# Optimization experiments

Hardware: AMD Instinct MI355X
Metric: run time of the kernel (lower is better)

## Reference

```python
import jax, jax.numpy as jnp
import numpy as np

OUT_DIM = 64
NUM_HEADS = 8
HID = NUM_HEADS * OUT_DIM  # 512
ALPHA = 0.01  # leaky relu slope
N_NODES = 20000
N_EDGES = 100000
MP_LEN = 3


def setup_inputs() -> dict:
    key = jax.random.key(0)
    ks = jax.random.split(key, 8)
    s = 1.0 / np.sqrt(HID)
    return {
        "features": jax.random.normal(ks[0], (N_NODES, OUT_DIM), jnp.float32),
        "W_ih": jax.random.normal(ks[1], (3 * HID, OUT_DIM), jnp.float32) * s,
        "W_hh": jax.random.normal(ks[2], (3 * HID, HID), jnp.float32) * s,
        "b_ih": jax.random.normal(ks[3], (3 * HID,), jnp.float32) * s,
        "b_hh": jax.random.normal(ks[4], (3 * HID,), jnp.float32) * s,
        "attn": jax.random.normal(ks[5], (NUM_HEADS, OUT_DIM), jnp.float32) * 0.1,
        "edge_metapath_indices": jax.random.randint(ks[6], (N_EDGES, MP_LEN), 0, N_NODES),
        "edge_dst": jax.random.randint(ks[7], (N_EDGES,), 0, N_NODES),
    }


def _gru_last_hidden(x_seq, W_ih, W_hh, b_ih, b_hh):
    """x_seq: [L, E, D] -> final hidden [E, HID] (torch nn.GRU math, h0=0)."""
    E = x_seq.shape[1]
    h0 = jnp.zeros((E, HID), x_seq.dtype)

    def step(h, x):
        gi = x @ W_ih.T + b_ih  # [E, 3*HID]
        gh = h @ W_hh.T + b_hh  # [E, 3*HID]
        i_r, i_z, i_n = jnp.split(gi, 3, axis=-1)
        h_r, h_z, h_n = jnp.split(gh, 3, axis=-1)
        r = jax.nn.sigmoid(i_r + h_r)
        z = jax.nn.sigmoid(i_z + h_z)
        n = jnp.tanh(i_n + r * h_n)
        h_new = (1.0 - z) * n + z * h
        return h_new, None

    h_last, _ = jax.lax.scan(step, h0, x_seq)
    return h_last


def reference(features, W_ih, W_hh, b_ih, b_hh, attn,
              edge_metapath_indices, edge_dst):
    N = features.shape[0]
    # gather metapath node features: [E, L, D] -> GRU over L
    edata = features[edge_metapath_indices]
    h = _gru_last_hidden(jnp.transpose(edata, (1, 0, 2)), W_ih, W_hh, b_ih, b_hh)
    eft = h.reshape(-1, NUM_HEADS, OUT_DIM)  # [E, H, D]
    # attention logits per edge/head + leaky relu
    a = jnp.sum(eft * attn[None], axis=-1)  # [E, H]
    a = jnp.where(a >= 0, a, ALPHA * a)
    # edge softmax grouped by destination node
    amax = jax.ops.segment_max(a, edge_dst, num_segments=N)  # [N, H]
    ea = jnp.exp(a - amax[edge_dst])
    denom = jax.ops.segment_sum(ea, edge_dst, num_segments=N)  # [N, H]
    alpha = ea / denom[edge_dst]  # [E, H]
    # weighted message aggregation (sum) to destination nodes
    msg = eft * alpha[:, :, None]  # [E, H, D]
    ret = jax.ops.segment_sum(msg, edge_dst, num_segments=N)  # [N, H, D]
    return ret
```

## Files before the change

### kernel.cpp

```cpp
#include <hip/hip_runtime.h>
#include <hip/hip_bf16.h>

#define N_NODES 20000
#define N_EDGES 100000
#define HID 512
#define G3 1536
#define NH 8
#define OD 64

typedef __hip_bfloat16 bf16;
typedef __attribute__((ext_vector_type(8))) short bf16x8;
typedef __attribute__((ext_vector_type(4))) float f32x4;

__device__ __forceinline__ float frcp(float x) { return __builtin_amdgcn_rcpf(x); }
__device__ __forceinline__ float fsig(float x) { return frcp(1.0f + __expf(-x)); }
__device__ __forceinline__ float ftanh(float x) { return 1.0f - 2.0f * frcp(__expf(2.0f * x) + 1.0f); }
__device__ __forceinline__ float b2f(bf16 b) { return __bfloat162float(b); }
__device__ __forceinline__ bf16 f2b(float f) { return __float2bfloat16(f); }
__device__ __forceinline__ float bs2f(short s) {
    return __uint_as_float(((unsigned)(unsigned short)s) << 16);
}
__device__ __forceinline__ float us2f(unsigned short s) {
    return __uint_as_float(((unsigned)s) << 16);
}
__device__ __forceinline__ short f2bs(float f) {
    bf16 b = __float2bfloat16(f);
    return *reinterpret_cast<short*>(&b);
}
__device__ __forceinline__ unsigned ford(float f) {
    unsigned u = __float_as_uint(f);
    return (u & 0x80000000u) ? ~u : (u | 0x80000000u);
}
__device__ __forceinline__ float iford(unsigned u) {
    return __uint_as_float((u & 0x80000000u) ? (u & 0x7fffffffu) : ~u);
}

__device__ __forceinline__ void g2l16(const void* g, void* l) {
#if __has_builtin(__builtin_amdgcn_global_load_lds)
    __builtin_amdgcn_global_load_lds((const __attribute__((address_space(1))) char*)g,
                                     (__attribute__((address_space(3))) char*)l, 16, 0, 0);
#else
    *(bf16x8*)l = *(const bf16x8*)g;
#endif
}


__global__ __launch_bounds__(256) void k_prep(const float* __restrict__ Whh,
                                              const float* __restrict__ Wih,
                                              bf16* __restrict__ WTs,
                                              float* __restrict__ WIT) {
    int t = blockIdx.x * 256 + threadIdx.x;
    if (t < 98304) {
        int T = t >> 10, c = (t >> 6) & 15, l = t & 63;
        int n = T * 16 + (l & 15);
        int k = c * 32 + ((l >> 4) << 3);
        const float* src = Whh + (size_t)n * 512 + k;
        bf16x8 v;
#pragma unroll
        for (int j = 0; j < 8; ++j) v[j] = f2bs(src[j]);
        *(bf16x8*)(WTs + (size_t)t * 8) = v;
    } else {
        int u = t - 98304;
        int d = u / 1536, j = u % 1536;
        WIT[u] = Wih[(size_t)j * 64 + d];
    }
}

__global__ __launch_bounds__(256) void k_count(const int* __restrict__ dst,
                                               unsigned* __restrict__ cnt) {
    int e = blockIdx.x * 256 + threadIdx.x;
    if (e < N_EDGES) atomicAdd(&cnt[dst[e]], 1u);
}

#define SCAN_CH 79
__global__ __launch_bounds__(256) void k_scan(const unsigned* __restrict__ cnt,
                                              unsigned* __restrict__ base,
                                              unsigned* __restrict__ cursor) {
    __shared__ unsigned ls[256];
    int t = threadIdx.x;
    int s0 = t * SCAN_CH;
    int s1 = s0 + SCAN_CH < N_NODES ? s0 + SCAN_CH : N_NODES;
    unsigned s = 0;
    for (int i = s0; i < s1; ++i) s += cnt[i];
    ls[t] = s;
    __syncthreads();
    for (int d = 1; d < 256; d <<= 1) {
        unsigned v = (t >= d) ? ls[t - d] : 0u;
        __syncthreads();
        ls[t] += v;
        __syncthreads();
    }
    unsigned run = ls[t] - s;
    for (int i = s0; i < s1; ++i) {
        base[i] = run; cursor[i] = run; run += cnt[i];
    }
    if (t == 255) base[N_NODES] = ls[255];
}

__global__ __launch_bounds__(256) void k_fill(const int* __restrict__ dst,
                                              unsigned* __restrict__ cursor,
                                              unsigned* __restrict__ csr) {
    int e = blockIdx.x * 256 + threadIdx.x;
    if (e < N_EDGES) {
        unsigned p = atomicAdd(&cursor[dst[e]], 1u);
        csr[p] = (unsigned)e;
    }
}

__global__ __launch_bounds__(256) void k_gi(const float* __restrict__ feat,
                                            const float* __restrict__ WIT,
                                            const float* __restrict__ b_ih,
                                            const float* __restrict__ b_hh,
                                            bf16* __restrict__ G,
                                            bf16* __restrict__ H1) {
    __shared__ float fs[16][64];
    const int n0 = blockIdx.x * 16;
    const int k = blockIdx.y * 256 + threadIdx.x;
    for (int i = threadIdx.x; i < 16 * 64; i += 256)
        fs[0][i] = feat[(size_t)n0 * 64 + i];
    __syncthreads();
    float acc[3][16];
#pragma unroll
    for (int g = 0; g < 3; ++g) {
        float b = b_ih[g * 512 + k];
#pragma unroll
        for (int e = 0; e < 16; ++e) acc[g][e] = b;
    }
    for (int d = 0; d < 64; d += 4) {
        float w[3][4];
#pragma unroll
        for (int u = 0; u < 4; ++u)
#pragma unroll
            for (int g = 0; g < 3; ++g)
                w[g][u] = WIT[(size_t)(d + u) * G3 + g * 512 + k];
#pragma unroll
        for (int e = 0; e < 16; ++e) {
            float4 f = *(const float4*)&fs[e][d];
#pragma unroll
            for (int g = 0; g < 3; ++g)
                acc[g][e] += w[g][0] * f.x + w[g][1] * f.y + w[g][2] * f.z + w[g][3] * f.w;
        }
    }
    const float br = b_hh[k], bz = b_hh[512 + k], bn = b_hh[1024 + k];
#pragma unroll
    for (int e = 0; e < 16; ++e) {
        bf16* dst = G + (size_t)(n0 + e) * G3 + k * 3;
        dst[0] = f2b(acc[0][e]);
        dst[1] = f2b(acc[1][e]);
        dst[2] = f2b(acc[2][e]);
        float r1 = fsig(acc[0][e] + br);
        float z1 = fsig(acc[1][e] + bz);
        float n1 = ftanh(acc[2][e] + r1 * bn);
        H1[(size_t)(n0 + e) * HID + k] = f2b((1.0f - z1) * n1);
    }
}

__global__ __launch_bounds__(256, 2) void k_gh2(const bf16* __restrict__ H1,
                                                const bf16* __restrict__ WTs,
                                                const float* __restrict__ b_hh,
                                                bf16* __restrict__ GH2) {
    __shared__ short Bs[2][8192];
    const int tid = threadIdx.x;
    const int wave = tid >> 6, lane = tid & 63;
    const int m0 = blockIdx.x * 128;
    const int k0 = (lane >> 4) << 3;

    bf16x8 afrag[2][16];
#pragma unroll
    for (int t = 0; t < 2; ++t) {
        int row = m0 + wave * 32 + t * 16 + (lane & 15);
        int ar = row < N_NODES ? row : N_NODES - 1;
#pragma unroll
        for (int c = 0; c < 16; ++c)
            afrag[t][c] = *(const bf16x8*)(H1 + (size_t)ar * HID + c * 32 + k0);
    }

    const int col = lane & 15;
    const int qb = (lane >> 4) << 2;
    const int boff = lane * 8;

#pragma unroll
    for (int i = 0; i < 4; ++i) {
        int q = tid + i * 256;
        g2l16(WTs + (size_t)q * 8, &Bs[0][q * 8]);
    }
    __syncthreads();

    int cur = 0;
    for (int jt = 0; jt < 32; ++jt) {
        const int cj = jt * 16 + col;
        f32x4 acc[2][3];
#pragma unroll
        for (int t = 0; t < 2; ++t)
#pragma unroll
            for (int g = 0; g < 3; ++g) acc[t][g] = (f32x4){0, 0, 0, 0};
        const float br = b_hh[cj], bz = b_hh[512 + cj], bn = b_hh[1024 + cj];
        {
#pragma unroll
            for (int i = 0; i < 4; ++i) {
                int q = tid + i * 256;
                g2l16(WTs + 262144 + (size_t)jt * 8192 + q * 8, &Bs[cur ^ 1][q * 8]);
            }
            const short* cb = &Bs[cur][0];
#pragma unroll
            for (int c = 0; c < 16; ++c) {
                bf16x8 b = *(const bf16x8*)&cb[c * 512 + boff];
                acc[0][0] = __builtin_amdgcn_mfma_f32_16x16x32_bf16(afrag[0][c], b, acc[0][0], 0, 0, 0);
                acc[1][0] = __builtin_amdgcn_mfma_f32_16x16x32_bf16(afrag[1][c], b, acc[1][0], 0, 0, 0);
            }
            __syncthreads();
            cur ^= 1;
        }
        {
#pragma unroll
            for (int i = 0; i < 4; ++i) {
                int q = tid + i * 256;
                g2l16(WTs + 524288 + (size_t)jt * 8192 + q * 8, &Bs[cur ^ 1][q * 8]);
            }
            const short* cb = &Bs[cur][0];
#pragma unroll
            for (int c = 0; c < 16; ++c) {
                bf16x8 b = *(const bf16x8*)&cb[c * 512 + boff];
                acc[0][1] = __builtin_amdgcn_mfma_f32_16x16x32_bf16(afrag[0][c], b, acc[0][1], 0, 0, 0);
                acc[1][1] = __builtin_amdgcn_mfma_f32_16x16x32_bf16(afrag[1][c], b, acc[1][1], 0, 0, 0);
            }
            __syncthreads();
            cur ^= 1;
        }
        {
            if (jt < 31) {
#pragma unroll
                for (int i = 0; i < 4; ++i) {
                    int q = tid + i * 256;
                    g2l16(WTs + (size_t)(jt + 1) * 8192 + q * 8, &Bs[cur ^ 1][q * 8]);
                }
            }
            const short* cb = &Bs[cur][0];
#pragma unroll
            for (int c = 0; c < 16; ++c) {
                bf16x8 b = *(const bf16x8*)&cb[c * 512 + boff];
                acc[0][2] = __builtin_amdgcn_mfma_f32_16x16x32_bf16(afrag[0][c], b, acc[0][2], 0, 0, 0);
                acc[1][2] = __builtin_amdgcn_mfma_f32_16x16x32_bf16(afrag[1][c], b, acc[1][2], 0, 0, 0);
            }
#pragma unroll
            for (int t = 0; t < 2; ++t)
#pragma unroll
                for (int q = 0; q < 4; ++q) {
                    int e = m0 + wave * 32 + t * 16 + qb + q;
                    if (e < N_NODES) {
                        bf16* dst = GH2 + (size_t)e * G3 + cj * 3;
                        dst[0] = f2b(acc[t][0][q] + br);
                        dst[1] = f2b(acc[t][1][q] + bz);
                        dst[2] = f2b(acc[t][2][q] + bn);
                    }
                }
            __syncthreads();
            cur ^= 1;
        }
    }
}

__global__ __launch_bounds__(256) void k_h2(const bf16* __restrict__ G,
                                            const bf16* __restrict__ GH2,
                                            const bf16* __restrict__ H1,
                                            const int* __restrict__ emi,
                                            bf16* __restrict__ h2) {
    size_t i = (size_t)blockIdx.x * 256 + threadIdx.x;
    int e = (int)(i >> 6);
    int kc = (int)(i & 63) * 8;
    int i0 = emi[(size_t)e * 3 + 0];
    int i1 = emi[(size_t)e * 3 + 1];
    const bf16* g1p = G + (size_t)i1 * G3 + kc * 3;
    const bf16* ghp = GH2 + (size_t)i0 * G3 + kc * 3;
    bf16x8 h1v = *(const bf16x8*)(H1 + (size_t)i0 * HID + kc);
    short s1[24], sh[24];
    {
        bf16x8 a0 = *(const bf16x8*)g1p, a1 = *(const bf16x8*)(g1p + 8), a2 = *(const bf16x8*)(g1p + 16);
        bf16x8 c0 = *(const bf16x8*)ghp, c1 = *(const bf16x8*)(ghp + 8), c2 = *(const bf16x8*)(ghp + 16);
#pragma unroll
        for (int j = 0; j < 8; ++j) {
            s1[j] = a0[j]; s1[8 + j] = a1[j]; s1[16 + j] = a2[j];
            sh[j] = c0[j]; sh[8 + j] = c1[j]; sh[16 + j] = c2[j];
        }
    }
    bf16x8 out;
#pragma unroll
    for (int j = 0; j < 8; ++j) {
        float r = fsig(bs2f(s1[j * 3 + 0]) + bs2f(sh[j * 3 + 0]));
        float z = fsig(bs2f(s1[j * 3 + 1]) + bs2f(sh[j * 3 + 1]));
        float n = ftanh(bs2f(s1[j * 3 + 2]) + r * bs2f(sh[j * 3 + 2]));
        out[j] = f2bs((1.0f - z) * n + z * bs2f(h1v[j]));
    }
    *(bf16x8*)(h2 + (size_t)e * HID + kc) = out;
}

__global__ __launch_bounds__(256, 2) void k_gemm3(const bf16* __restrict__ G,
                                                  const bf16* __restrict__ WTs,
                                                  const float* __restrict__ b_hh,
                                                  const int* __restrict__ emi,
                                                  bf16* __restrict__ h2) {
    __shared__ short Bs[2][8192];
    __shared__ int si2[128];
    const int tid = threadIdx.x;
    const int wave = tid >> 6, lane = tid & 63;
    const int m0 = blockIdx.x * 128;
    if (tid < 128) {
        int e = m0 + tid;
        si2[tid] = emi[(size_t)(e < N_EDGES ? e : N_EDGES - 1) * 3 + 2];
    }
    const int k0 = (lane >> 4) << 3;

    bf16x8 afrag[2][16];
#pragma unroll
    for (int t = 0; t < 2; ++t) {
        int row = m0 + wave * 32 + t * 16 + (lane & 15);
        int ar = row < N_EDGES ? row : N_EDGES - 1;
#pragma unroll
        for (int c = 0; c < 16; ++c)
            afrag[t][c] = *(const bf16x8*)(h2 + (size_t)ar * HID + c * 32 + k0);
    }

    const int col = lane & 15;
    const int qb = (lane >> 4) << 2;
    const int boff = lane * 8;

#pragma unroll
    for (int i = 0; i < 4; ++i) {
        int q = tid + i * 256;
        g2l16(WTs + (size_t)q * 8, &Bs[0][q * 8]);
    }
    __syncthreads();

    int cur = 0;
    for (int jt = 0; jt < 32; ++jt) {
        const int cj = jt * 16 + col;
        f32x4 acc[2][3];
#pragma unroll
        for (int t = 0; t < 2; ++t)
#pragma unroll
            for (int g = 0; g < 3; ++g) acc[t][g] = (f32x4){0, 0, 0, 0};
        float br, bz, bn;
        unsigned short pg[2][4][3], ph[2][4];
        {
            br = b_hh[cj]; bz = b_hh[512 + cj]; bn = b_hh[1024 + cj];
#pragma unroll
            for (int t = 0; t < 2; ++t)
#pragma unroll
                for (int q = 0; q < 4; ++q) {
                    int li = wave * 32 + t * 16 + qb + q;
                    int e = m0 + li;
                    int ec = e < N_EDGES ? e : N_EDGES - 1;
                    const unsigned short* g2p =
                        (const unsigned short*)(G + (size_t)si2[li] * G3 + cj * 3);
                    pg[t][q][0] = g2p[0]; pg[t][q][1] = g2p[1]; pg[t][q][2] = g2p[2];
                    ph[t][q] = ((const unsigned short*)h2)[(size_t)ec * HID + cj];
                }
#pragma unroll
            for (int i = 0; i < 4; ++i) {
                int q = tid + i * 256;
                g2l16(WTs + 262144 + (size_t)jt * 8192 + q * 8, &Bs[cur ^ 1][q * 8]);
            }
            const short* cb = &Bs[cur][0];
#pragma unroll
            for (int c = 0; c < 16; ++c) {
                bf16x8 b = *(const bf16x8*)&cb[c * 512 + boff];
                acc[0][0] = __builtin_amdgcn_mfma_f32_16x16x32_bf16(afrag[0][c], b, acc[0][0], 0, 0, 0);
                acc[1][0] = __builtin_amdgcn_mfma_f32_16x16x32_bf16(afrag[1][c], b, acc[1][0], 0, 0, 0);
            }
            __syncthreads();
            cur ^= 1;
        }
        {
#pragma unroll
            for (int i = 0; i < 4; ++i) {
                int q = tid + i * 256;
                g2l16(WTs + 524288 + (size_t)jt * 8192 + q * 8, &Bs[cur ^ 1][q * 8]);
            }
            const short* cb = &Bs[cur][0];
#pragma unroll
            for (int c = 0; c < 16; ++c) {
                bf16x8 b = *(const bf16x8*)&cb[c * 512 + boff];
                acc[0][1] = __builtin_amdgcn_mfma_f32_16x16x32_bf16(afrag[0][c], b, acc[0][1], 0, 0, 0);
                acc[1][1] = __builtin_amdgcn_mfma_f32_16x16x32_bf16(afrag[1][c], b, acc[1][1], 0, 0, 0);
            }
            __syncthreads();
            cur ^= 1;
        }
        {
            if (jt < 31) {
#pragma unroll
                for (int i = 0; i < 4; ++i) {
                    int q = tid + i * 256;
                    g2l16(WTs + (size_t)(jt + 1) * 8192 + q * 8, &Bs[cur ^ 1][q * 8]);
                }
            }
            const short* cb = &Bs[cur][0];
#pragma unroll
            for (int c = 0; c < 16; ++c) {
                bf16x8 b = *(const bf16x8*)&cb[c * 512 + boff];
                acc[0][2] = __builtin_amdgcn_mfma_f32_16x16x32_bf16(afrag[0][c], b, acc[0][2], 0, 0, 0);
                acc[1][2] = __builtin_amdgcn_mfma_f32_16x16x32_bf16(afrag[1][c], b, acc[1][2], 0, 0, 0);
            }
#pragma unroll
            for (int t = 0; t < 2; ++t)
#pragma unroll
                for (int q = 0; q < 4; ++q) {
                    int e = m0 + wave * 32 + t * 16 + qb + q;
                    if (e < N_EDGES) {
                        float r = fsig(us2f(pg[t][q][0]) + acc[t][0][q] + br);
                        float z = fsig(us2f(pg[t][q][1]) + acc[t][1][q] + bz);
                        float ng = ftanh(us2f(pg[t][q][2]) + r * (acc[t][2][q] + bn));
                        h2[(size_t)e * HID + cj] = f2b((1.0f - z) * ng + z * us2f(ph[t][q]));
                    }
                }
            __syncthreads();
            cur ^= 1;
        }
    }
}

__global__ __launch_bounds__(256) void k_logits(const bf16* __restrict__ eft,
                                                const float* __restrict__ attn,
                                                const int* __restrict__ dst,
                                                float* __restrict__ a,
                                                unsigned* __restrict__ amax) {
    int i = blockIdx.x * 256 + threadIdx.x;
    int e = i >> 3, h = i & 7;
    const __hip_bfloat162* f2 = (const __hip_bfloat162*)(eft + (size_t)e * HID + h * OD);
    const float* at = attn + h * OD;
    float s = 0.f;
#pragma unroll
    for (int d = 0; d < OD / 2; ++d) {
        float2 fv = __bfloat1622float2(f2[d]);
        s += fv.x * at[2 * d] + fv.y * at[2 * d + 1];
    }
    s = (s >= 0.f) ? s : 0.01f * s;
    a[i] = s;
    atomicMax(&amax[(size_t)dst[e] * NH + h], ford(s));
}

__global__ __launch_bounds__(256) void k_ea(const int* __restrict__ dst,
                                            const unsigned* __restrict__ amax,
                                            float* __restrict__ a,
                                            float* __restrict__ denom) {
    int i = blockIdx.x * 256 + threadIdx.x;
    int e = i >> 3, h = i & 7;
    float m = iford(amax[(size_t)dst[e] * NH + h]);
    float v = __expf(a[i] - m);
    a[i] = v;
    atomicAdd(&denom[(size_t)dst[e] * NH + h], v);
}

__global__ __launch_bounds__(256) void k_out(const bf16* __restrict__ eft,
                                             const float* __restrict__ a,
                                             const float* __restrict__ denom,
                                             const unsigned* __restrict__ base,
                                             const unsigned* __restrict__ csr,
                                             float* __restrict__ out) {
    int n = blockIdx.x;
    int k = blockIdx.y * 256 + threadIdx.x;
    int h = k >> 6;
    unsigned b0 = base[n], b1 = base[n + 1];
    float rden = (b1 > b0) ? frcp(denom[(size_t)n * NH + h]) : 0.0f;
    float acc = 0.f;
    for (unsigned i = b0; i < b1; ++i) {
        unsigned e = csr[i];
        float al = a[(size_t)e * NH + h];
        acc += b2f(eft[(size_t)e * HID + k]) * al;
    }
    out[(size_t)n * HID + k] = acc * rden;
}

extern "C" void kernel_launch(void* const* d_in, const int* in_sizes, int n_in,
                              void* d_out, int out_size, void* d_ws, size_t ws_size,
                              hipStream_t stream) {
    (void)in_sizes; (void)n_in; (void)ws_size; (void)out_size;
    const float* feat = (const float*)d_in[0];
    const float* W_ih = (const float*)d_in[1];
    const float* W_hh = (const float*)d_in[2];
    const float* b_ih = (const float*)d_in[3];
    const float* b_hh = (const float*)d_in[4];
    const float* attn = (const float*)d_in[5];
    const int* emi = (const int*)d_in[6];
    const int* dst = (const int*)d_in[7];
    float* out = (float*)d_out;

    char* ws = (char*)d_ws;
    bf16* G = (bf16*)ws;
    bf16* GH2 = (bf16*)(ws + 61440000);
    bf16* h2 = (bf16*)(ws + 122880000);
    bf16* WTs = (bf16*)(ws + 225280000);
    float* WIT = (float*)(ws + 226852864);
    float* a = (float*)(ws + 227246080);
    unsigned* amax = (unsigned*)(ws + 230446080);
    float* denom = (float*)(ws + 231086080);
    unsigned* cnt = (unsigned*)(ws + 231726080);
    unsigned* base = (unsigned*)(ws + 231806080);
    unsigned* cursor = (unsigned*)(ws + 231886088);
    unsigned* csr = (unsigned*)(ws + 231966088);
    bf16* H1 = (bf16*)(ws + 232366088);

    (void)hipMemsetAsync(amax, 0, 1360000, stream);

    k_prep<<<768, 256, 0, stream>>>(W_hh, W_ih, WTs, WIT);
    k_count<<<391, 256, 0, stream>>>(dst, cnt);
    k_scan<<<1, 256, 0, stream>>>(cnt, base, cursor);
    k_fill<<<391, 256, 0, stream>>>(dst, cursor, csr);
    k_gi<<<dim3(1250, 2), 256, 0, stream>>>(feat, WIT, b_ih, b_hh, G, H1);
    k_gh2<<<157, 256, 0, stream>>>(H1, WTs, b_hh, GH2);
    k_h2<<<25000, 256, 0, stream>>>(G, GH2, H1, emi, h2);
    k_gemm3<<<782, 256, 0, stream>>>(G, WTs, b_hh, emi, h2);
    k_logits<<<3125, 256, 0, stream>>>(h2, attn, dst, a, amax);
    k_ea<<<3125, 256, 0, stream>>>(dst, amax, a, denom);
    k_out<<<dim3(N_NODES, 2), 256, 0, stream>>>(h2, a, denom, base, csr, out);
}
```

Before: 801.4 us.

## Fuse input-gate GEMM into final GRU step and shrink tile to 64 rows

The third GRU step no longer gathers its precomputed input-gate values from the G table. It now computes x@W_ih on the fly with two extra MFMAs per gate, using bf16 copies of the features and of a swizzled W_ih prepared in k_prep. The per-block edge tile drops from 128 to 64 rows and the occupancy hint rises from 2 to 3 blocks, which reduces register pressure from the A fragments. In exchange there is extra MFMA work and B-tile reloads are amortised over fewer rows, while the scattered 2-byte gathers from the large G table go away.

```diff
diff --git a/kernel.cpp b/kernel.cpp
--- a/kernel.cpp
+++ b/kernel.cpp
@@ -47,7 +47,10 @@
 
 __global__ __launch_bounds__(256) void k_prep(const float* __restrict__ Whh,
                                               const float* __restrict__ Wih,
+                                              const float* __restrict__ feat,
                                               bf16* __restrict__ WTs,
+                                              bf16* __restrict__ WIE,
+                                              bf16* __restrict__ featB,
                                               float* __restrict__ WIT) {
     int t = blockIdx.x * 256 + threadIdx.x;
     if (t < 98304) {
@@ -59,10 +62,27 @@
 #pragma unroll
         for (int j = 0; j < 8; ++j) v[j] = f2bs(src[j]);
         *(bf16x8*)(WTs + (size_t)t * 8) = v;
-    } else {
+    } else if (t < 196608) {
         int u = t - 98304;
         int d = u / 1536, j = u % 1536;
         WIT[u] = Wih[(size_t)j * 64 + d];
+    } else if (t < 208896) {
+        int u = t - 196608;
+        int l = u & 63, cc = (u >> 6) & 1, jt = (u >> 7) & 31, g = u >> 12;
+        int row = g * 512 + jt * 16 + (l & 15);
+        int d0 = cc * 32 + ((l >> 4) << 3);
+        const float* src = Wih + (size_t)row * 64 + d0;
+        bf16x8 v;
+#pragma unroll
+        for (int j = 0; j < 8; ++j) v[j] = f2bs(src[j]);
+        *(bf16x8*)(WIE + (size_t)u * 8) = v;
+    } else {
+        int u = t - 208896;
+        const float* src = feat + (size_t)u * 8;
+        bf16x8 v;
+#pragma unroll
+        for (int j = 0; j < 8; ++j) v[j] = f2bs(src[j]);
+        *(bf16x8*)(featB + (size_t)u * 8) = v;
     }
 }
 
@@ -294,32 +314,23 @@
     *(bf16x8*)(h2 + (size_t)e * HID + kc) = out;
 }
 
-__global__ __launch_bounds__(256, 2) void k_gemm3(const bf16* __restrict__ G,
+__global__ __launch_bounds__(256, 3) void k_gemm3(const bf16* __restrict__ featB,
                                                   const bf16* __restrict__ WTs,
+                                                  const bf16* __restrict__ WIE,
+                                                  const float* __restrict__ b_ih,
                                                   const float* __restrict__ b_hh,
                                                   const int* __restrict__ emi,
                                                   bf16* __restrict__ h2) {
-    __shared__ short Bs[2][8192];
-    __shared__ int si2[128];
+    __shared__ short Bs[2][9216];
+    __shared__ int si2[64];
     const int tid = threadIdx.x;
     const int wave = tid >> 6, lane = tid & 63;
-    const int m0 = blockIdx.x * 128;
-    if (tid < 128) {
+    const int m0 = blockIdx.x * 64;
+    if (tid < 64) {
         int e = m0 + tid;
         si2[tid] = emi[(size_t)(e < N_EDGES ? e : N_EDGES - 1) * 3 + 2];
     }
     const int k0 = (lane >> 4) << 3;
-
-    bf16x8 afrag[2][16];
-#pragma unroll
-    for (int t = 0; t < 2; ++t) {
-        int row = m0 + wave * 32 + t * 16 + (lane & 15);
-        int ar = row < N_EDGES ? row : N_EDGES - 1;
-#pragma unroll
-        for (int c = 0; c < 16; ++c)
-            afrag[t][c] = *(const bf16x8*)(h2 + (size_t)ar * HID + c * 32 + k0);
-    }
-
     const int col = lane & 15;
     const int qb = (lane >> 4) << 2;
     const int boff = lane * 8;
@@ -329,43 +340,55 @@
         int q = tid + i * 256;
         g2l16(WTs + (size_t)q * 8, &Bs[0][q * 8]);
     }
+    if (tid < 128) g2l16(WIE + (size_t)tid * 8, &Bs[0][8192 + tid * 8]);
     __syncthreads();
+
+    bf16x8 afrag[18];
+    {
+        int row = m0 + wave * 16 + (lane & 15);
+        int ar = row < N_EDGES ? row : N_EDGES - 1;
+#pragma unroll
+        for (int c = 0; c < 16; ++c)
+            afrag[c] = *(const bf16x8*)(h2 + (size_t)ar * HID + c * 32 + k0);
+        int i2r = si2[wave * 16 + (lane & 15)];
+        afrag[16] = *(const bf16x8*)(featB + (size_t)i2r * 64 + k0);
+        afrag[17] = *(const bf16x8*)(featB + (size_t)i2r * 64 + 32 + k0);
+    }
 
     int cur = 0;
     for (int jt = 0; jt < 32; ++jt) {
         const int cj = jt * 16 + col;
-        f32x4 acc[2][3];
-#pragma unroll
-        for (int t = 0; t < 2; ++t)
-#pragma unroll
-            for (int g = 0; g < 3; ++g) acc[t][g] = (f32x4){0, 0, 0, 0};
-        float br, bz, bn;
-        unsigned short pg[2][4][3], ph[2][4];
+        f32x4 ar_ = {0, 0, 0, 0}, az_ = {0, 0, 0, 0};
+        f32x4 ahn = {0, 0, 0, 0}, ain = {0, 0, 0, 0};
+        float bihr, bihz, bihn, bhhr, bhhz, bhhn;
+        unsigned short ph[4];
         {
-            br = b_hh[cj]; bz = b_hh[512 + cj]; bn = b_hh[1024 + cj];
-#pragma unroll
-            for (int t = 0; t < 2; ++t)
-#pragma unroll
-                for (int q = 0; q < 4; ++q) {
-                    int li = wave * 32 + t * 16 + qb + q;
-                    int e = m0 + li;
-                    int ec = e < N_EDGES ? e : N_EDGES - 1;
-                    const unsigned short* g2p =
-                        (const unsigned short*)(G + (size_t)si2[li] * G3 + cj * 3);
-                    pg[t][q][0] = g2p[0]; pg[t][q][1] = g2p[1]; pg[t][q][2] = g2p[2];
-                    ph[t][q] = ((const unsigned short*)h2)[(size_t)ec * HID + cj];
-                }
+            bihr = b_ih[cj]; bihz = b_ih[512 + cj]; bihn = b_ih[1024 + cj];
+            bhhr = b_hh[cj]; bhhz = b_hh[512 + cj]; bhhn = b_hh[1024 + cj];
+#pragma unroll
+            for (int q = 0; q < 4; ++q) {
+                int e = m0 + wave * 16 + qb + q;
+                int ec = e < N_EDGES ? e : N_EDGES - 1;
+                ph[q] = ((const unsigned short*)h2)[(size_t)ec * HID + cj];
+            }
 #pragma unroll
             for (int i = 0; i < 4; ++i) {
                 int q = tid + i * 256;
                 g2l16(WTs + 262144 + (size_t)jt * 8192 + q * 8, &Bs[cur ^ 1][q * 8]);
             }
+            if (tid < 128)
+                g2l16(WIE + 32768 + (size_t)jt * 1024 + tid * 8, &Bs[cur ^ 1][8192 + tid * 8]);
             const short* cb = &Bs[cur][0];
 #pragma unroll
             for (int c = 0; c < 16; ++c) {
                 bf16x8 b = *(const bf16x8*)&cb[c * 512 + boff];
-                acc[0][0] = __builtin_amdgcn_mfma_f32_16x16x32_bf16(afrag[0][c], b, acc[0][0], 0, 0, 0);
-                acc[1][0] = __builtin_amdgcn_mfma_f32_16x16x32_bf16(afrag[1][c], b, acc[1][0], 0, 0, 0);
+                ar_ = __builtin_amdgcn_mfma_f32_16x16x32_bf16(afrag[c], b, ar_, 0, 0, 0);
+            }
+            {
+                bf16x8 b16 = *(const bf16x8*)&cb[8192 + boff];
+                bf16x8 b17 = *(const bf16x8*)&cb[8192 + 512 + boff];
+                ar_ = __builtin_amdgcn_mfma_f32_16x16x32_bf16(afrag[16], b16, ar_, 0, 0, 0);
+                ar_ = __builtin_amdgcn_mfma_f32_16x16x32_bf16(afrag[17], b17, ar_, 0, 0, 0);
             }
             __syncthreads();
             cur ^= 1;
@@ -376,12 +399,19 @@
                 int q = tid + i * 256;
                 g2l16(WTs + 524288 + (size_t)jt * 8192 + q * 8, &Bs[cur ^ 1][q * 8]);
             }
+            if (tid < 128)
+                g2l16(WIE + 65536 + (size_t)jt * 1024 + tid * 8, &Bs[cur ^ 1][8192 + tid * 8]);
             const short* cb = &Bs[cur][0];
 #pragma unroll
             for (int c = 0; c < 16; ++c) {
                 bf16x8 b = *(const bf16x8*)&cb[c * 512 + boff];
-                acc[0][1] = __builtin_amdgcn_mfma_f32_16x16x32_bf16(afrag[0][c], b, acc[0][1], 0, 0, 0);
-                acc[1][1] = __builtin_amdgcn_mfma_f32_16x16x32_bf16(afrag[1][c], b, acc[1][1], 0, 0, 0);
+                az_ = __builtin_amdgcn_mfma_f32_16x16x32_bf16(afrag[c], b, az_, 0, 0, 0);
+            }
+            {
+                bf16x8 b16 = *(const bf16x8*)&cb[8192 + boff];
+                bf16x8 b17 = *(const bf16x8*)&cb[8192 + 512 + boff];
+                az_ = __builtin_amdgcn_mfma_f32_16x16x32_bf16(afrag[16], b16, az_, 0, 0, 0);
+                az_ = __builtin_amdgcn_mfma_f32_16x16x32_bf16(afrag[17], b17, az_, 0, 0, 0);
             }
             __syncthreads();
             cur ^= 1;
@@ -393,26 +423,31 @@
                     int q = tid + i * 256;
                     g2l16(WTs + (size_t)(jt + 1) * 8192 + q * 8, &Bs[cur ^ 1][q * 8]);
                 }
+                if (tid < 128)
+                    g2l16(WIE + (size_t)(jt + 1) * 1024 + tid * 8, &Bs[cur ^ 1][8192 + tid * 8]);
             }
             const short* cb = &Bs[cur][0];
 #pragma unroll
             for (int c = 0; c < 16; ++c) {
                 bf16x8 b = *(const bf16x8*)&cb[c * 512 + boff];
-                acc[0][2] = __builtin_amdgcn_mfma_f32_16x16x32_bf16(afrag[0][c], b, acc[0][2], 0, 0, 0);
-                acc[1][2] = __builtin_amdgcn_mfma_f32_16x16x32_bf16(afrag[1][c], b, acc[1][2], 0, 0, 0);
-            }
-#pragma unroll
-            for (int t = 0; t < 2; ++t)
-#pragma unroll
-                for (int q = 0; q < 4; ++q) {
-                    int e = m0 + wave * 32 + t * 16 + qb + q;
-                    if (e < N_EDGES) {
-                        float r = fsig(us2f(pg[t][q][0]) + acc[t][0][q] + br);
-                        float z = fsig(us2f(pg[t][q][1]) + acc[t][1][q] + bz);
-                        float ng = ftanh(us2f(pg[t][q][2]) + r * (acc[t][2][q] + bn));
-                        h2[(size_t)e * HID + cj] = f2b((1.0f - z) * ng + z * us2f(ph[t][q]));
-                    }
+                ahn = __builtin_amdgcn_mfma_f32_16x16x32_bf16(afrag[c], b, ahn, 0, 0, 0);
+            }
+            {
+                bf16x8 b16 = *(const bf16x8*)&cb[8192 + boff];
+                bf16x8 b17 = *(const bf16x8*)&cb[8192 + 512 + boff];
+                ain = __builtin_amdgcn_mfma_f32_16x16x32_bf16(afrag[16], b16, ain, 0, 0, 0);
+                ain = __builtin_amdgcn_mfma_f32_16x16x32_bf16(afrag[17], b17, ain, 0, 0, 0);
+            }
+#pragma unroll
+            for (int q = 0; q < 4; ++q) {
+                int e = m0 + wave * 16 + qb + q;
+                if (e < N_EDGES) {
+                    float r = fsig(ar_[q] + bihr + bhhr);
+                    float z = fsig(az_[q] + bihz + bhhz);
+                    float n = ftanh(ain[q] + bihn + r * (ahn[q] + bhhn));
+                    h2[(size_t)e * HID + cj] = f2b((1.0f - z) * n + z * us2f(ph[q]));
                 }
+            }
             __syncthreads();
             cur ^= 1;
         }
@@ -499,17 +534,19 @@
     unsigned* cursor = (unsigned*)(ws + 231886088);
     unsigned* csr = (unsigned*)(ws + 231966088);
     bf16* H1 = (bf16*)(ws + 232366088);
+    bf16* WIE = (bf16*)(ws + 227246080);
+    bf16* featB = (bf16*)(ws + 227442688);
 
     (void)hipMemsetAsync(amax, 0, 1360000, stream);
 
-    k_prep<<<768, 256, 0, stream>>>(W_hh, W_ih, WTs, WIT);
+    k_prep<<<1441, 256, 0, stream>>>(W_hh, W_ih, feat, WTs, WIE, featB, WIT);
     k_count<<<391, 256, 0, stream>>>(dst, cnt);
     k_scan<<<1, 256, 0, stream>>>(cnt, base, cursor);
     k_fill<<<391, 256, 0, stream>>>(dst, cursor, csr);
     k_gi<<<dim3(1250, 2), 256, 0, stream>>>(feat, WIT, b_ih, b_hh, G, H1);
     k_gh2<<<157, 256, 0, stream>>>(H1, WTs, b_hh, GH2);
     k_h2<<<25000, 256, 0, stream>>>(G, GH2, H1, emi, h2);
-    k_gemm3<<<782, 256, 0, stream>>>(G, WTs, b_hh, emi, h2);
+    k_gemm3<<<1563, 256, 0, stream>>>(featB, WTs, WIE, b_ih, b_hh, emi, h2);
     k_logits<<<3125, 256, 0, stream>>>(h2, attn, dst, a, amax);
     k_ea<<<3125, 256, 0, stream>>>(dst, amax, a, denom);
     k_out<<<dim3(N_NODES, 2), 256, 0, stream>>>(h2, a, denom, base, csr, out);
```

After: 788.6 us. Within noise of the previous version (-1.6%).

## Restructure final GRU GEMM to keep weights resident and fuse input projection

Applied to the files above, without the earlier changes.

The third-step GEMM now gives each block a fixed 16-column slice of all three gates, keeps those W_hh and W_ih tiles resident in LDS, and loops over 33 row tiles. The input projection is computed inline with MFMA from bf16 features instead of reading the precomputed G buffer. Output goes to a separate buffer so h2 stays unchanged, and blocks are mapped to XCDs for L2 locality. The GH2 kernel now stages outputs through LDS so it can issue coalesced 16-byte stores. The cost is more LDS per block, a larger A-fragment register set, and bf16 rounding of the input projection.

```diff
diff --git a/kernel.cpp b/kernel.cpp
--- a/kernel.cpp
+++ b/kernel.cpp
@@ -47,7 +47,10 @@
 
 __global__ __launch_bounds__(256) void k_prep(const float* __restrict__ Whh,
                                               const float* __restrict__ Wih,
+                                              const float* __restrict__ feat,
                                               bf16* __restrict__ WTs,
+                                              bf16* __restrict__ WIE,
+                                              bf16* __restrict__ featB,
                                               float* __restrict__ WIT) {
     int t = blockIdx.x * 256 + threadIdx.x;
     if (t < 98304) {
@@ -59,10 +62,28 @@
 #pragma unroll
         for (int j = 0; j < 8; ++j) v[j] = f2bs(src[j]);
         *(bf16x8*)(WTs + (size_t)t * 8) = v;
-    } else {
+    } else if (t < 196608) {
         int u = t - 98304;
         int d = u / 1536, j = u % 1536;
         WIT[u] = Wih[(size_t)j * 64 + d];
+    } else if (t < 208896) {
+        int u = t - 196608;
+        int l = u & 63, cc = (u >> 6) & 1, jg = u >> 7;
+        int jt = jg & 31, g = jg >> 5;
+        int row = g * 512 + jt * 16 + (l & 15);
+        int d0 = cc * 32 + ((l >> 4) << 3);
+        const float* src = Wih + (size_t)row * 64 + d0;
+        bf16x8 v;
+#pragma unroll
+        for (int j = 0; j < 8; ++j) v[j] = f2bs(src[j]);
+        *(bf16x8*)(WIE + (size_t)u * 8) = v;
+    } else {
+        int u = t - 208896;
+        const float* src = feat + (size_t)u * 8;
+        bf16x8 v;
+#pragma unroll
+        for (int j = 0; j < 8; ++j) v[j] = f2bs(src[j]);
+        *(bf16x8*)(featB + (size_t)u * 8) = v;
     }
 }
 
@@ -160,6 +181,7 @@
                                                 const float* __restrict__ b_hh,
                                                 bf16* __restrict__ GH2) {
     __shared__ short Bs[2][8192];
+    __shared__ short tile2[128 * 48];
     const int tid = threadIdx.x;
     const int wave = tid >> 6, lane = tid & 63;
     const int m0 = blockIdx.x * 128;
@@ -196,6 +218,17 @@
             for (int g = 0; g < 3; ++g) acc[t][g] = (f32x4){0, 0, 0, 0};
         const float br = b_hh[cj], bz = b_hh[512 + cj], bn = b_hh[1024 + cj];
         {
+            if (jt > 0) {
+                int pj = jt - 1;
+#pragma unroll
+                for (int i_ = 0; i_ < 3; ++i_) {
+                    int idx = i_ * 256 + tid;
+                    int rg = m0 + (idx / 6);
+                    if (rg < N_NODES)
+                        *(bf16x8*)(GH2 + (size_t)rg * G3 + pj * 48 + (idx % 6) * 8) =
+                            *(const bf16x8*)&tile2[idx * 8];
+                }
+            }
 #pragma unroll
             for (int i = 0; i < 4; ++i) {
                 int q = tid + i * 256;
@@ -246,17 +279,23 @@
             for (int t = 0; t < 2; ++t)
 #pragma unroll
                 for (int q = 0; q < 4; ++q) {
-                    int e = m0 + wave * 32 + t * 16 + qb + q;
-                    if (e < N_NODES) {
-                        bf16* dst = GH2 + (size_t)e * G3 + cj * 3;
-                        dst[0] = f2b(acc[t][0][q] + br);
-                        dst[1] = f2b(acc[t][1][q] + bz);
-                        dst[2] = f2b(acc[t][2][q] + bn);
-                    }
+                    int lr = wave * 32 + t * 16 + qb + q;
+                    short* s = &tile2[lr * 48 + col * 3];
+                    s[0] = f2bs(acc[t][0][q] + br);
+                    s[1] = f2bs(acc[t][1][q] + bz);
+                    s[2] = f2bs(acc[t][2][q] + bn);
                 }
             __syncthreads();
             cur ^= 1;
         }
+    }
+#pragma unroll
+    for (int i_ = 0; i_ < 3; ++i_) {
+        int idx = i_ * 256 + tid;
+        int rg = m0 + (idx / 6);
+        if (rg < N_NODES)
+            *(bf16x8*)(GH2 + (size_t)rg * G3 + 31 * 48 + (idx % 6) * 8) =
+                *(const bf16x8*)&tile2[idx * 8];
     }
 }
 
@@ -294,128 +333,111 @@
     *(bf16x8*)(h2 + (size_t)e * HID + kc) = out;
 }
 
-__global__ __launch_bounds__(256, 2) void k_gemm3(const bf16* __restrict__ G,
+__global__ __launch_bounds__(256, 2) void k_gemm3(const bf16* __restrict__ featB,
                                                   const bf16* __restrict__ WTs,
+                                                  const bf16* __restrict__ WIE,
+                                                  const float* __restrict__ b_ih,
                                                   const float* __restrict__ b_hh,
                                                   const int* __restrict__ emi,
-                                                  bf16* __restrict__ h2) {
-    __shared__ short Bs[2][8192];
-    __shared__ int si2[128];
+                                                  const bf16* __restrict__ h2,
+                                                  bf16* __restrict__ h3out) {
+    __shared__ short Ws[3][8192];
+    __shared__ short We[3][1024];
     const int tid = threadIdx.x;
     const int wave = tid >> 6, lane = tid & 63;
-    const int m0 = blockIdx.x * 128;
-    if (tid < 128) {
-        int e = m0 + tid;
-        si2[tid] = emi[(size_t)(e < N_EDGES ? e : N_EDGES - 1) * 3 + 2];
-    }
+    const int bid = blockIdx.x;
+    const int xcd = bid & 7, sl = bid >> 3;
+    const int mt = xcd * 3 + (sl >> 5);
+    const int cg = sl & 31;
+    const int mbase = mt * 4224;
+    const int col = lane & 15;
+    const int cj = cg * 16 + col;
     const int k0 = (lane >> 4) << 3;
-
-    bf16x8 afrag[2][16];
-#pragma unroll
-    for (int t = 0; t < 2; ++t) {
-        int row = m0 + wave * 32 + t * 16 + (lane & 15);
-        int ar = row < N_EDGES ? row : N_EDGES - 1;
-#pragma unroll
-        for (int c = 0; c < 16; ++c)
-            afrag[t][c] = *(const bf16x8*)(h2 + (size_t)ar * HID + c * 32 + k0);
-    }
-
-    const int col = lane & 15;
     const int qb = (lane >> 4) << 2;
     const int boff = lane * 8;
 
 #pragma unroll
-    for (int i = 0; i < 4; ++i) {
-        int q = tid + i * 256;
-        g2l16(WTs + (size_t)q * 8, &Bs[0][q * 8]);
-    }
+    for (int g = 0; g < 3; ++g) {
+#pragma unroll
+        for (int i = 0; i < 4; ++i) {
+            int q = tid + i * 256;
+            g2l16(WTs + (size_t)g * 262144 + (size_t)cg * 8192 + q * 8, &Ws[g][q * 8]);
+        }
+        if (tid < 128)
+            g2l16(WIE + (size_t)g * 32768 + (size_t)cg * 1024 + tid * 8, &We[g][tid * 8]);
+    }
+    const float rb = b_ih[cj] + b_hh[cj];
+    const float zb = b_ih[512 + cj] + b_hh[512 + cj];
+    const float nb = b_ih[1024 + cj];
+    const float hb = b_hh[1024 + cj];
     __syncthreads();
 
-    int cur = 0;
-    for (int jt = 0; jt < 32; ++jt) {
-        const int cj = jt * 16 + col;
-        f32x4 acc[2][3];
+    for (int st = 0; st < 33; ++st) {
+        const int rowb = mbase + st * 128 + wave * 32;
+        bf16x8 af[2][18];
+#pragma unroll
+        for (int t = 0; t < 2; ++t) {
+            int row = rowb + t * 16 + (lane & 15);
+            int ar = row < N_EDGES ? row : N_EDGES - 1;
+#pragma unroll
+            for (int c = 0; c < 16; ++c)
+                af[t][c] = *(const bf16x8*)(h2 + (size_t)ar * HID + c * 32 + k0);
+            int i2 = emi[(size_t)ar * 3 + 2];
+            af[t][16] = *(const bf16x8*)(featB + (size_t)i2 * 64 + k0);
+            af[t][17] = *(const bf16x8*)(featB + (size_t)i2 * 64 + 32 + k0);
+        }
+        unsigned short ph[2][4];
 #pragma unroll
         for (int t = 0; t < 2; ++t)
 #pragma unroll
-            for (int g = 0; g < 3; ++g) acc[t][g] = (f32x4){0, 0, 0, 0};
-        float br, bz, bn;
-        unsigned short pg[2][4][3], ph[2][4];
-        {
-            br = b_hh[cj]; bz = b_hh[512 + cj]; bn = b_hh[1024 + cj];
-#pragma unroll
-            for (int t = 0; t < 2; ++t)
-#pragma unroll
-                for (int q = 0; q < 4; ++q) {
-                    int li = wave * 32 + t * 16 + qb + q;
-                    int e = m0 + li;
-                    int ec = e < N_EDGES ? e : N_EDGES - 1;
-                    const unsigned short* g2p =
-                        (const unsigned short*)(G + (size_t)si2[li] * G3 + cj * 3);
-                    pg[t][q][0] = g2p[0]; pg[t][q][1] = g2p[1]; pg[t][q][2] = g2p[2];
-                    ph[t][q] = ((const unsigned short*)h2)[(size_t)ec * HID + cj];
+            for (int q = 0; q < 4; ++q) {
+                int row = rowb + t * 16 + qb + q;
+                int ec = row < N_EDGES ? row : N_EDGES - 1;
+                ph[t][q] = ((const unsigned short*)h2)[(size_t)ec * HID + cj];
+            }
+        f32x4 ar_[2], az_[2], ahn[2], ain[2];
+#pragma unroll
+        for (int t = 0; t < 2; ++t) {
+            ar_[t] = (f32x4){0, 0, 0, 0}; az_[t] = (f32x4){0, 0, 0, 0};
+            ahn[t] = (f32x4){0, 0, 0, 0}; ain[t] = (f32x4){0, 0, 0, 0};
+        }
+#pragma unroll
+        for (int c = 0; c < 16; ++c) {
+            bf16x8 br = *(const bf16x8*)&Ws[0][c * 512 + boff];
+            bf16x8 bz = *(const bf16x8*)&Ws[1][c * 512 + boff];
+            bf16x8 bn = *(const bf16x8*)&Ws[2][c * 512 + boff];
+#pragma unroll
+            for (int t = 0; t < 2; ++t) {
+                ar_[t] = __builtin_amdgcn_mfma_f32_16x16x32_bf16(af[t][c], br, ar_[t], 0, 0, 0);
+                az_[t] = __builtin_amdgcn_mfma_f32_16x16x32_bf16(af[t][c], bz, az_[t], 0, 0, 0);
+                ahn[t] = __builtin_amdgcn_mfma_f32_16x16x32_bf16(af[t][c], bn, ahn[t], 0, 0, 0);
+            }
+        }
+#pragma unroll
+        for (int cc = 0; cc < 2; ++cc) {
+            bf16x8 br = *(const bf16x8*)&We[0][cc * 512 + boff];
+            bf16x8 bz = *(const bf16x8*)&We[1][cc * 512 + boff];
+            bf16x8 bn = *(const bf16x8*)&We[2][cc * 512 + boff];
+#pragma unroll
+            for (int t = 0; t < 2; ++t) {
+                ar_[t] = __builtin_amdgcn_mfma_f32_16x16x32_bf16(af[t][16 + cc], br, ar_[t], 0, 0, 0);
+                az_[t] = __builtin_amdgcn_mfma_f32_16x16x32_bf16(af[t][16 + cc], bz, az_[t], 0, 0, 0);
+                ain[t] = __builtin_amdgcn_mfma_f32_16x16x32_bf16(af[t][16 + cc], bn, ain[t], 0, 0, 0);
+            }
+        }
+#pragma unroll
+        for (int t = 0; t < 2; ++t)
+#pragma unroll
+            for (int q = 0; q < 4; ++q) {
+                int row = rowb + t * 16 + qb + q;
+                if (row < N_EDGES) {
+                    float r = fsig(ar_[t][q] + rb);
+                    float z = fsig(az_[t][q] + zb);
+                    float n = ftanh(ain[t][q] + nb + r * (ahn[t][q] + hb));
+                    h3out[(size_t)row * HID + cj] =
+                        f2b((1.0f - z) * n + z * us2f(ph[t][q]));
                 }
-#pragma unroll
-            for (int i = 0; i < 4; ++i) {
-                int q = tid + i * 256;
-                g2l16(WTs + 262144 + (size_t)jt * 8192 + q * 8, &Bs[cur ^ 1][q * 8]);
-            }
-            const short* cb = &Bs[cur][0];
-#pragma unroll
-            for (int c = 0; c < 16; ++c) {
-                bf16x8 b = *(const bf16x8*)&cb[c * 512 + boff];
-                acc[0][0] = __builtin_amdgcn_mfma_f32_16x16x32_bf16(afrag[0][c], b, acc[0][0], 0, 0, 0);
-                acc[1][0] = __builtin_amdgcn_mfma_f32_16x16x32_bf16(afrag[1][c], b, acc[1][0], 0, 0, 0);
-            }
-            __syncthreads();
-            cur ^= 1;
-        }
-        {
-#pragma unroll
-            for (int i = 0; i < 4; ++i) {
-                int q = tid + i * 256;
-                g2l16(WTs + 524288 + (size_t)jt * 8192 + q * 8, &Bs[cur ^ 1][q * 8]);
-            }
-            const short* cb = &Bs[cur][0];
-#pragma unroll
-            for (int c = 0; c < 16; ++c) {
-                bf16x8 b = *(const bf16x8*)&cb[c * 512 + boff];
-                acc[0][1] = __builtin_amdgcn_mfma_f32_16x16x32_bf16(afrag[0][c], b, acc[0][1], 0, 0, 0);
-                acc[1][1] = __builtin_amdgcn_mfma_f32_16x16x32_bf16(afrag[1][c], b, acc[1][1], 0, 0, 0);
-            }
-            __syncthreads();
-            cur ^= 1;
-        }
-        {
-            if (jt < 31) {
-#pragma unroll
-                for (int i = 0; i < 4; ++i) {
-                    int q = tid + i * 256;
-                    g2l16(WTs + (size_t)(jt + 1) * 8192 + q * 8, &Bs[cur ^ 1][q * 8]);
-                }
-            }
-            const short* cb = &Bs[cur][0];
-#pragma unroll
-            for (int c = 0; c < 16; ++c) {
-                bf16x8 b = *(const bf16x8*)&cb[c * 512 + boff];
-                acc[0][2] = __builtin_amdgcn_mfma_f32_16x16x32_bf16(afrag[0][c], b, acc[0][2], 0, 0, 0);
-                acc[1][2] = __builtin_amdgcn_mfma_f32_16x16x32_bf16(afrag[1][c], b, acc[1][2], 0, 0, 0);
-            }
-#pragma unroll
-            for (int t = 0; t < 2; ++t)
-#pragma unroll
-                for (int q = 0; q < 4; ++q) {
-                    int e = m0 + wave * 32 + t * 16 + qb + q;
-                    if (e < N_EDGES) {
-                        float r = fsig(us2f(pg[t][q][0]) + acc[t][0][q] + br);
-                        float z = fsig(us2f(pg[t][q][1]) + acc[t][1][q] + bz);
-                        float ng = ftanh(us2f(pg[t][q][2]) + r * (acc[t][2][q] + bn));
-                        h2[(size_t)e * HID + cj] = f2b((1.0f - z) * ng + z * us2f(ph[t][q]));
-                    }
-                }
-            __syncthreads();
-            cur ^= 1;
-        }
+            }
     }
 }
 
@@ -499,18 +521,21 @@
     unsigned* cursor = (unsigned*)(ws + 231886088);
     unsigned* csr = (unsigned*)(ws + 231966088);
     bf16* H1 = (bf16*)(ws + 232366088);
+    bf16* WIE = (bf16*)(ws + 227246080);
+    bf16* featB = (bf16*)(ws + 227442688);
+    bf16* h3out = (bf16*)ws;
 
     (void)hipMemsetAsync(amax, 0, 1360000, stream);
 
-    k_prep<<<768, 256, 0, stream>>>(W_hh, W_ih, WTs, WIT);
+    k_prep<<<1441, 256, 0, stream>>>(W_hh, W_ih, feat, WTs, WIE, featB, WIT);
     k_count<<<391, 256, 0, stream>>>(dst, cnt);
     k_scan<<<1, 256, 0, stream>>>(cnt, base, cursor);
     k_fill<<<391, 256, 0, stream>>>(dst, cursor, csr);
     k_gi<<<dim3(1250, 2), 256, 0, stream>>>(feat, WIT, b_ih, b_hh, G, H1);
     k_gh2<<<157, 256, 0, stream>>>(H1, WTs, b_hh, GH2);
     k_h2<<<25000, 256, 0, stream>>>(G, GH2, H1, emi, h2);
-    k_gemm3<<<782, 256, 0, stream>>>(G, WTs, b_hh, emi, h2);
-    k_logits<<<3125, 256, 0, stream>>>(h2, attn, dst, a, amax);
+    k_gemm3<<<768, 256, 0, stream>>>(featB, WTs, WIE, b_ih, b_hh, emi, h2, h3out);
+    k_logits<<<3125, 256, 0, stream>>>(h3out, attn, dst, a, amax);
     k_ea<<<3125, 256, 0, stream>>>(dst, amax, a, denom);
-    k_out<<<dim3(N_NODES, 2), 256, 0, stream>>>(h2, a, denom, base, csr, out);
-}
+    k_out<<<dim3(N_NODES, 2), 256, 0, stream>>>(h3out, a, denom, base, csr, out);
+}
```

Result: slower. 1.155 ms (+44.2%).
